# Optimization experiments

Hardware: AMD Instinct MI355X
Metric: run time of the kernel (lower is better)

## Reference

```python
import jax, jax.numpy as jnp
import numpy as np

E = 1024
H = 16
HD = E // H


def _shift(pos_score):
    # Transformer-XL relative shift trick. pos_score: [B,H,Q,K]
    B, nH, Q, K = pos_score.shape
    zeros = jnp.zeros((B, nH, Q, 1), pos_score.dtype)
    padded = jnp.concatenate([zeros, pos_score], axis=-1)  # [B,H,Q,K+1]
    padded = padded.reshape(B, nH, K + 1, Q)
    return padded[:, :, 1:].reshape(B, nH, Q, K)


def setup_inputs() -> dict:
    key = jax.random.key(0)
    ks = jax.random.split(key, 14)
    B, S = 2, 1024
    s = 1.0 / np.sqrt(E)
    inp = {
        "query": jax.random.normal(ks[0], (B, S, E), jnp.float32),
        "key": jax.random.normal(ks[1], (B, S, E), jnp.float32),
        "value": jax.random.normal(ks[2], (B, S, E), jnp.float32),
        "pos_embedding": jax.random.normal(ks[3], (B, S, E), jnp.float32),
        "Wq": jax.random.normal(ks[4], (E, E), jnp.float32) * s,
        "bq": jnp.zeros((E,), jnp.float32),
        "Wk": jax.random.normal(ks[5], (E, E), jnp.float32) * s,
        "bk": jnp.zeros((E,), jnp.float32),
        "Wv": jax.random.normal(ks[6], (E, E), jnp.float32) * s,
        "bv": jnp.zeros((E,), jnp.float32),
        "Wp": jax.random.normal(ks[7], (E, E), jnp.float32) * s,
        "U": jax.random.normal(ks[8], (H, HD), jnp.float32) * s,
        "V": jax.random.normal(ks[9], (H, HD), jnp.float32) * s,
        "Wo": jax.random.normal(ks[10], (E, E), jnp.float32) * s,
        "bo": jnp.zeros((E,), jnp.float32),
    }
    return inp


def reference(query, key, value, pos_embedding, Wq, bq, Wk, bk, Wv, bv, Wp, U, V, Wo, bo):
    B, Q, _ = query.shape
    K = key.shape[1]
    d = jnp.asarray(np.sqrt(E), query.dtype)

    q = (query @ Wq + bq).reshape(B, Q, H, HD)
    k = (key @ Wk + bk).reshape(B, K, H, HD)
    v = (value @ Wv + bv).reshape(B, K, H, HD)
    R = (pos_embedding @ Wp).reshape(B, -1, H, HD)

    content_score = jnp.einsum('bqhd,bkhd->bhqk', q + U, k)
    position_score = jnp.einsum('bqhd,bkhd->bhqk', q + V, R)
    position_score = _shift(position_score)
    attention_score = (content_score + position_score) / d  # no softmax in original

    # NOTE: faithful to original einsum 'bhqk,bvhd->bqhd' where k and v are
    # both contracted independently (sums scores over k, values over v).
    alpha = jnp.einsum('bhqk,bvhd->bqhd', attention_score, v).reshape(B, Q, E)
    return alpha @ Wo + bo
```

## Files before the change

kernel.cpp:

```cpp
#include <hip/hip_runtime.h>
#include <cstddef>
#include <cstdint>

#define E_ 1024
#define H_ 16
#define HD_ 64
#define B_ 2
#define S_ 1024
#define NSEG 64
#define SEGLEN (S_/NSEG)
#define CHUNKS 64
#define CHLEN (S_/CHUNKS)
#define SCALE 0.03125f

typedef __attribute__((ext_vector_type(8))) short bf16x8;
typedef __attribute__((ext_vector_type(4))) float f32x4;

__device__ __forceinline__ unsigned short f2bf_rne(float x) {
  uint32_t u = __float_as_uint(x);
  uint32_t r = u + 0x7FFFu + ((u >> 16) & 1u);
  return (unsigned short)(r >> 16);
}
__device__ __forceinline__ float bf2f(unsigned short h) {
  return __uint_as_float(((uint32_t)h) << 16);
}
__device__ __forceinline__ void gload_lds16(const void* g, void* l) {
  __builtin_amdgcn_global_load_lds(
      (const __attribute__((address_space(1))) void*)g,
      (__attribute__((address_space(3))) void*)l, 16, 0, 0);
}

__global__ __launch_bounds__(256) void kA_segsum(
    const float* __restrict__ pos, float* __restrict__ seg) {
  int idx = blockIdx.x*256 + threadIdx.x;
  int e = idx % E_;
  int g = (idx / E_) % NSEG;
  int b = idx / (E_*NSEG);
  const float* p = pos + ((size_t)(b*S_ + g*SEGLEN))*E_ + e;
  float s = 0.f;
  #pragma unroll
  for (int i = 0; i < SEGLEN; ++i) s += p[(size_t)i*E_];
  seg[(b*NSEG + g)*E_ + e] = s;
}

__global__ __launch_bounds__(256) void kB_scan_split(
    const float* __restrict__ pos, const float* __restrict__ seg,
    unsigned short* __restrict__ Ap) {
  int idx = blockIdx.x*256 + threadIdx.x;
  int e = idx % E_;
  int g = (idx / E_) % NSEG;
  int b = idx / (E_*NSEG);
  float run = 0.f;
  for (int gp = 0; gp < g; ++gp) run += seg[(b*NSEG + gp)*E_ + e];
  const float* p = pos + ((size_t)(b*S_ + g*SEGLEN))*E_ + e;
  #pragma unroll
  for (int i = 0; i < SEGLEN; ++i) {
    run += p[(size_t)i*E_];
    size_t row = (size_t)(b*S_ + g*SEGLEN + i);
    unsigned short hb = f2bf_rne(run);
    float lf = run - bf2f(hb);
    Ap[row*2048 + e]        = hb;
    Ap[row*2048 + 1024 + e] = f2bf_rne(lf);
  }
}

__global__ __launch_bounds__(256) void kC_split_q(
    const float* __restrict__ q, unsigned short* __restrict__ Aq) {
  int idx = blockIdx.x*256 + threadIdx.x;
  int e4 = idx & 255;
  int r  = idx >> 8;
  float4 v = ((const float4*)q)[idx];
  float xs[4] = {v.x, v.y, v.z, v.w};
  ushort4 hi, lo;
  unsigned short hb; float lf;
  hb = f2bf_rne(xs[0]); lf = xs[0]-bf2f(hb); hi.x = hb; lo.x = f2bf_rne(lf);
  hb = f2bf_rne(xs[1]); lf = xs[1]-bf2f(hb); hi.y = hb; lo.y = f2bf_rne(lf);
  hb = f2bf_rne(xs[2]); lf = xs[2]-bf2f(hb); hi.z = hb; lo.z = f2bf_rne(lf);
  hb = f2bf_rne(xs[3]); lf = xs[3]-bf2f(hb); hi.w = hb; lo.w = f2bf_rne(lf);
  *(ushort4*)&Aq[(size_t)r*2048 + e4*4]        = hi;
  *(ushort4*)&Aq[(size_t)r*2048 + 1024 + e4*4] = lo;
}

__global__ __launch_bounds__(256) void kD_splitW(
    const float* __restrict__ Wq, const float* __restrict__ Wp,
    unsigned short* __restrict__ Btq, unsigned short* __restrict__ Btp) {
  __shared__ float tile[32][33];
  const float* W = blockIdx.z ? Wp : Wq;
  unsigned short* Bt = blockIdx.z ? Btp : Btq;
  int nt = blockIdx.x, kt = blockIdx.y;
  int t = threadIdx.x;
  int lr = t >> 3;
  int lc = (t & 7) * 4;
  float4 v = *(const float4*)&W[(size_t)(kt*32 + lr)*E_ + nt*32 + lc];
  tile[lr][lc+0] = v.x; tile[lr][lc+1] = v.y;
  tile[lr][lc+2] = v.z; tile[lr][lc+3] = v.w;
  __syncthreads();
  int n = nt*32 + lr;
  ushort4 hi, lo;
  unsigned short hb; float lf; float x;
  x = tile[lc+0][lr]; hb = f2bf_rne(x); lf = x-bf2f(hb); hi.x = hb; lo.x = f2bf_rne(lf);
  x = tile[lc+1][lr]; hb = f2bf_rne(x); lf = x-bf2f(hb); hi.y = hb; lo.y = f2bf_rne(lf);
  x = tile[lc+2][lr]; hb = f2bf_rne(x); lf = x-bf2f(hb); hi.z = hb; lo.z = f2bf_rne(lf);
  x = tile[lc+3][lr]; hb = f2bf_rne(x); lf = x-bf2f(hb); hi.w = hb; lo.w = f2bf_rne(lf);
  *(ushort4*)&Bt[(size_t)n*2048 + kt*32 + lc]        = hi;
  *(ushort4*)&Bt[(size_t)n*2048 + 1024 + kt*32 + lc] = lo;
}

__global__ __launch_bounds__(256) void k1_colsum_partial(
    const float* __restrict__ key, const float* __restrict__ value,
    float* __restrict__ pk, float* __restrict__ pv) {
  int idx = blockIdx.x*256 + threadIdx.x;
  int e = idx % E_;
  int c = (idx / E_) % CHUNKS;
  int b = idx / (E_*CHUNKS);
  const float* kp = key   + ((size_t)(b*S_ + c*CHLEN))*E_ + e;
  const float* vp = value + ((size_t)(b*S_ + c*CHLEN))*E_ + e;
  float sk = 0.f, sv = 0.f;
  #pragma unroll
  for (int s = 0; s < CHLEN; ++s) {
    sk += kp[(size_t)s*E_];
    sv += vp[(size_t)s*E_];
  }
  pk[(b*CHUNKS + c)*E_ + e] = sk;
  pv[(b*CHUNKS + c)*E_ + e] = sv;
}

__global__ __launch_bounds__(256) void k2a_colsum(
    const float* __restrict__ pk, const float* __restrict__ pv,
    float* __restrict__ colsum) {
  int idx = blockIdx.x*256 + threadIdx.x;
  int e = idx & 1023;
  int b = (idx >> 10) & 1;
  int j = idx >> 11;
  const float* p = j ? pv : pk;
  float s = 0.f;
  #pragma unroll 8
  for (int c = 0; c < CHUNKS; ++c) s += p[(b*CHUNKS + c)*E_ + e];
  colsum[idx] = s;
}

__global__ __launch_bounds__(256) void k2b_gemv(
    const float* __restrict__ colsum, const float* __restrict__ Wk,
    const float* __restrict__ Wv, float* __restrict__ partial) {
  int j     = blockIdx.z;
  int slice = blockIdx.y;
  int n     = blockIdx.x*256 + threadIdx.x;
  const float* W  = j ? Wv : Wk;
  const float* cs = colsum + j*2048;
  float a0 = 0.f, a1 = 0.f;
  int e0 = slice*64;
  #pragma unroll 8
  for (int i = 0; i < 64; ++i) {
    int e = e0 + i;
    float w = W[(size_t)e*E_ + n];
    a0 += cs[e] * w;
    a1 += cs[1024 + e] * w;
  }
  partial[(size_t)((j*16 + slice)*2 + 0)*E_ + n] = a0;
  partial[(size_t)((j*16 + slice)*2 + 1)*E_ + n] = a1;
}

__global__ __launch_bounds__(256) void k2c_reduce(
    const float* __restrict__ partial, const float* __restrict__ bk,
    const float* __restrict__ bv, float* __restrict__ ksum,
    float* __restrict__ vsum) {
  int idx = blockIdx.x*256 + threadIdx.x;
  int n = idx & 1023;
  int b = (idx >> 10) & 1;
  int j = idx >> 11;
  const float* base = partial + (size_t)(j*32 + b)*E_ + n;
  float s = 0.f;
  #pragma unroll
  for (int sl = 0; sl < 16; ++sl) s += base[(size_t)sl*2*E_];
  s += (float)S_ * (j ? bv[n] : bk[n]);
  (j ? vsum : ksum)[b*E_ + n] = s;
}

__global__ __launch_bounds__(256) void k3_wv(
    const float* __restrict__ vsum, const float* __restrict__ Wo,
    float* __restrict__ WV) {
  int idx = blockIdx.x*256 + threadIdx.x;
  int n = idx % E_;
  int h = (idx / E_) % H_;
  int b = idx / (E_*H_);
  float acc = 0.f;
  #pragma unroll 8
  for (int d = 0; d < HD_; ++d)
    acc += vsum[b*E_ + h*HD_ + d] * Wo[(size_t)(h*HD_ + d)*E_ + n];
  WV[idx] = acc;
}

#define GNT 48
__global__ __launch_bounds__(256, 2) void kG_gemm(
    const unsigned short* __restrict__ Aq, const unsigned short* __restrict__ Btq,
    const float* __restrict__ bq,
    const unsigned short* __restrict__ Ap, const unsigned short* __restrict__ Btp,
    float* __restrict__ Cq, float* __restrict__ Cp) {
  __shared__ __align__(128) char lds[49152];
  const int t = threadIdx.x;
  const int lane = t & 63;
  const int wm = (t >> 6) >> 1;
  const int wn = (t >> 6) & 1;
  const int bn = blockIdx.x, bm = blockIdx.y;

  const unsigned short* A; const unsigned short* Bt;
  const float* bias; float* C;
  if (blockIdx.z == 0) { A = Aq; Bt = Btq; bias = bq;      C = Cq; }
  else                 { A = Ap; Bt = Btp; bias = nullptr; C = Cp; }

  const unsigned short* asrc[4];
  const unsigned short* bsrc[2];
  #pragma unroll
  for (int i = 0; i < 4; ++i) {
    int L = i*4096 + t*16;
    int row = L >> 7, bir = L & 127;
    int sw = bir ^ ((row & 7) << 4);
    asrc[i] = A + (size_t)(bm*128 + row)*2048 + (sw >> 1);
  }
  #pragma unroll
  for (int i = 0; i < 2; ++i) {
    int L = i*4096 + t*16;
    int row = L >> 7, bir = L & 127;
    int sw = bir ^ ((row & 7) << 4);
    bsrc[i] = Bt + (size_t)(bn*64 + row)*2048 + (sw >> 1);
  }
  int aoff[2][4], boff[2][2];
  #pragma unroll
  for (int ks = 0; ks < 2; ++ks) {
    int k0b = (ks*32 + (lane >> 4)*8) * 2;
    #pragma unroll
    for (int mi = 0; mi < 4; ++mi) {
      int row = wm*64 + mi*16 + (lane & 15);
      aoff[ks][mi] = row*128 + (k0b ^ ((row & 7) << 4));
    }
    #pragma unroll
    for (int ni = 0; ni < 2; ++ni) {
      int rown = wn*32 + ni*16 + (lane & 15);
      boff[ks][ni] = rown*128 + (k0b ^ ((rown & 7) << 4));
    }
  }

  f32x4 acc[4][2] = {};

  auto stage = [&](int buf, int kt) {
    int ak = (kt < 32) ? kt : kt - 32;
    int bk = (kt < 16) ? kt : kt - 16;
    char* Ab = lds + buf*16384;
    char* Bb = lds + 32768 + buf*8192;
    #pragma unroll
    for (int i = 0; i < 4; ++i)
      gload_lds16(asrc[i] + ak*64, Ab + i*4096 + t*16);
    #pragma unroll
    for (int i = 0; i < 2; ++i)
      gload_lds16(bsrc[i] + bk*64, Bb + i*4096 + t*16);
  };

  stage(0, 0);
  __syncthreads();
  int cur = 0;
  for (int kt = 0; kt < GNT; ++kt) {
    if (kt + 1 < GNT) stage(cur ^ 1, kt + 1);
    const char* Ab = lds + cur*16384;
    const char* Bb = lds + 32768 + cur*8192;
    bf16x8 af[2][4], bf_[2][2];
    #pragma unroll
    for (int ks = 0; ks < 2; ++ks) {
      #pragma unroll
      for (int mi = 0; mi < 4; ++mi)
        af[ks][mi] = *(const bf16x8*)(Ab + aoff[ks][mi]);
      #pragma unroll
      for (int ni = 0; ni < 2; ++ni)
        bf_[ks][ni] = *(const bf16x8*)(Bb + boff[ks][ni]);
    }
    #pragma unroll
    for (int ks = 0; ks < 2; ++ks)
      #pragma unroll
      for (int mi = 0; mi < 4; ++mi)
        #pragma unroll
        for (int ni = 0; ni < 2; ++ni)
          acc[mi][ni] = __builtin_amdgcn_mfma_f32_16x16x32_bf16(
              af[ks][mi], bf_[ks][ni], acc[mi][ni], 0, 0, 0);
    __syncthreads();
    cur ^= 1;
  }

  #pragma unroll
  for (int mi = 0; mi < 4; ++mi) {
    #pragma unroll
    for (int ni = 0; ni < 2; ++ni) {
      int col  = bn*64 + wn*32 + ni*16 + (lane & 15);
      int row0 = bm*128 + wm*64 + mi*16 + (lane >> 4)*4;
      float badd = bias ? bias[col] : 0.f;
      #pragma unroll
      for (int j = 0; j < 4; ++j)
        C[(size_t)(row0 + j)*E_ + col] = acc[mi][ni][j] + badd;
    }
  }
}

__global__ __launch_bounds__(256) void k6_rs(
    const float* __restrict__ qp, const float* __restrict__ Rpre,
    const float* __restrict__ ksum, const float* __restrict__ U,
    const float* __restrict__ V, float* __restrict__ rs) {
  int w    = blockIdx.x*4 + (threadIdx.x >> 6);
  int lane = threadIdx.x & 63;
  int q = w % S_;
  int h = (w / S_) % H_;
  int b = w / (S_*H_);
  int he = h*HD_ + lane;
  float qv0  = qp[((size_t)(b*S_ + q))*E_ + he];
  float u    = U[he], vv = V[he];
  float ks   = ksum[b*E_ + he];
  float rtot = Rpre[((size_t)(b*S_ + (S_-1)))*E_ + he];
  float tail = rtot;
  if (q <= S_-2) tail -= Rpre[((size_t)(b*S_ + (S_-2-q)))*E_ + he];
  float p = (qv0 + u)*ks + (qv0 + vv)*tail;
  if (q <= S_-3) {
    float qv1 = qp[((size_t)(b*S_ + q + 1))*E_ + he];
    float hd  = Rpre[((size_t)(b*S_ + (S_-3-q)))*E_ + he];
    p += (qv1 + vv)*hd;
  }
  #pragma unroll
  for (int off = 32; off >= 1; off >>= 1)
    p += __shfl_xor(p, off);
  if (lane == 0) rs[(b*H_ + h)*S_ + q] = p * SCALE;
}

__global__ __launch_bounds__(256) void k7_out(
    const float* __restrict__ rs, const float* __restrict__ WV,
    const float* __restrict__ bo, float* __restrict__ out) {
  int idx = blockIdx.x*256 + threadIdx.x;
  int n = idx % E_;
  int q = (idx / E_) % S_;
  int b = idx / (E_*S_);
  float acc = bo[n];
  #pragma unroll
  for (int h = 0; h < H_; ++h)
    acc += rs[(b*H_ + h)*S_ + q] * WV[((size_t)(b*H_ + h))*E_ + n];
  out[idx] = acc;
}

extern "C" void kernel_launch(void* const* d_in, const int* in_sizes, int n_in,
                              void* d_out, int out_size, void* d_ws, size_t ws_size,
                              hipStream_t stream) {
  const float* query = (const float*)d_in[0];
  const float* key   = (const float*)d_in[1];
  const float* value = (const float*)d_in[2];
  const float* pos   = (const float*)d_in[3];
  const float* Wq = (const float*)d_in[4];
  const float* bq = (const float*)d_in[5];
  const float* Wk = (const float*)d_in[6];
  const float* bk = (const float*)d_in[7];
  const float* Wv = (const float*)d_in[8];
  const float* bv = (const float*)d_in[9];
  const float* Wp = (const float*)d_in[10];
  const float* U  = (const float*)d_in[11];
  const float* V  = (const float*)d_in[12];
  const float* Wo = (const float*)d_in[13];
  const float* bo = (const float*)d_in[14];
  float* out = (float*)d_out;
  char* wsb = (char*)d_ws;

  unsigned short* Aqs = (unsigned short*)(wsb);
  unsigned short* Aps = (unsigned short*)(wsb + (8ull<<20));
  unsigned short* Btq = (unsigned short*)(wsb + (16ull<<20));
  unsigned short* Btp = (unsigned short*)(wsb + (20ull<<20));
  float* Rpre  = (float*)(wsb + (24ull<<20));
  char*  smallb = wsb + (32ull<<20);
  float* seg   = (float*)(smallb);
  float* pk    = (float*)(smallb + (512ull<<10));
  float* pv    = (float*)(smallb + (1024ull<<10));
  float* ksum  = (float*)(smallb + (1536ull<<10));
  float* vsum  = (float*)(smallb + (1544ull<<10));
  float* WVb   = (float*)(smallb + (1552ull<<10));
  float* rs    = (float*)(smallb + (1680ull<<10));
  float* qproj = out;
  float* colsum  = seg;
  float* partial = seg + 4096;

  hipLaunchKernelGGL(kA_segsum, dim3(B_*NSEG*E_/256), dim3(256), 0, stream, pos, seg);
  hipLaunchKernelGGL(kB_scan_split, dim3(B_*NSEG*E_/256), dim3(256), 0, stream, pos, seg, Aps);
  hipLaunchKernelGGL(kC_split_q, dim3(B_*S_*E_/4/256), dim3(256), 0, stream, query, Aqs);
  hipLaunchKernelGGL(kD_splitW, dim3(32, 32, 2), dim3(256), 0, stream, Wq, Wp, Btq, Btp);
  hipLaunchKernelGGL(k1_colsum_partial, dim3(B_*CHUNKS*E_/256), dim3(256), 0, stream,
                     key, value, pk, pv);
  hipLaunchKernelGGL(k2a_colsum, dim3(16), dim3(256), 0, stream, pk, pv, colsum);
  hipLaunchKernelGGL(k2b_gemv, dim3(4, 16, 2), dim3(256), 0, stream,
                     colsum, Wk, Wv, partial);
  hipLaunchKernelGGL(k2c_reduce, dim3(16), dim3(256), 0, stream,
                     partial, bk, bv, ksum, vsum);
  hipLaunchKernelGGL(k3_wv, dim3(B_*H_*E_/256), dim3(256), 0, stream, vsum, Wo, WVb);
  hipLaunchKernelGGL(kG_gemm, dim3(E_/64, B_*S_/128, 2), dim3(256), 0, stream,
                     Aqs, Btq, bq, Aps, Btp, qproj, Rpre);
  hipLaunchKernelGGL(k6_rs, dim3(B_*H_*S_/4), dim3(256), 0, stream,
                     qproj, Rpre, ksum, U, V, rs);
  hipLaunchKernelGGL(k7_out, dim3(B_*S_*E_/256), dim3(256), 0, stream,
                     rs, WVb, bo, out);
}
```

Measured before the change: 211.8 us.

## Merge independent preprocessing kernels into fused multi-role launches with atomic reduction

Collapses ten small launches into four by giving different block-index ranges different roles: segment sums, query split, weight split and key/value column sums share one launch, and scan plus colsum share another. The gemv partial reduction is replaced by atomicAdd into ksum/vsum, which are pre-initialised with the bias terms. The WV product is folded into the GEMM launch, and the GEMM block ids are remapped for locality. This removes launch gaps and serial dependencies, at the cost of nondeterministic atomic summation order and mixed-role blocks sharing one resource footprint.

```diff
diff --git a/kernel.cpp b/kernel.cpp
--- a/kernel.cpp
+++ b/kernel.cpp
@@ -30,121 +30,126 @@
       (__attribute__((address_space(3))) void*)l, 16, 0, 0);
 }
 
-__global__ __launch_bounds__(256) void kA_segsum(
-    const float* __restrict__ pos, float* __restrict__ seg) {
-  int idx = blockIdx.x*256 + threadIdx.x;
-  int e = idx % E_;
-  int g = (idx / E_) % NSEG;
-  int b = idx / (E_*NSEG);
-  const float* p = pos + ((size_t)(b*S_ + g*SEGLEN))*E_ + e;
-  float s = 0.f;
-  #pragma unroll
-  for (int i = 0; i < SEGLEN; ++i) s += p[(size_t)i*E_];
-  seg[(b*NSEG + g)*E_ + e] = s;
-}
-
-__global__ __launch_bounds__(256) void kB_scan_split(
-    const float* __restrict__ pos, const float* __restrict__ seg,
-    unsigned short* __restrict__ Ap) {
-  int idx = blockIdx.x*256 + threadIdx.x;
-  int e = idx % E_;
-  int g = (idx / E_) % NSEG;
-  int b = idx / (E_*NSEG);
-  float run = 0.f;
-  for (int gp = 0; gp < g; ++gp) run += seg[(b*NSEG + gp)*E_ + e];
-  const float* p = pos + ((size_t)(b*S_ + g*SEGLEN))*E_ + e;
-  #pragma unroll
-  for (int i = 0; i < SEGLEN; ++i) {
-    run += p[(size_t)i*E_];
-    size_t row = (size_t)(b*S_ + g*SEGLEN + i);
-    unsigned short hb = f2bf_rne(run);
-    float lf = run - bf2f(hb);
-    Ap[row*2048 + e]        = hb;
-    Ap[row*2048 + 1024 + e] = f2bf_rne(lf);
-  }
-}
-
-__global__ __launch_bounds__(256) void kC_split_q(
-    const float* __restrict__ q, unsigned short* __restrict__ Aq) {
-  int idx = blockIdx.x*256 + threadIdx.x;
-  int e4 = idx & 255;
-  int r  = idx >> 8;
-  float4 v = ((const float4*)q)[idx];
-  float xs[4] = {v.x, v.y, v.z, v.w};
-  ushort4 hi, lo;
-  unsigned short hb; float lf;
-  hb = f2bf_rne(xs[0]); lf = xs[0]-bf2f(hb); hi.x = hb; lo.x = f2bf_rne(lf);
-  hb = f2bf_rne(xs[1]); lf = xs[1]-bf2f(hb); hi.y = hb; lo.y = f2bf_rne(lf);
-  hb = f2bf_rne(xs[2]); lf = xs[2]-bf2f(hb); hi.z = hb; lo.z = f2bf_rne(lf);
-  hb = f2bf_rne(xs[3]); lf = xs[3]-bf2f(hb); hi.w = hb; lo.w = f2bf_rne(lf);
-  *(ushort4*)&Aq[(size_t)r*2048 + e4*4]        = hi;
-  *(ushort4*)&Aq[(size_t)r*2048 + 1024 + e4*4] = lo;
-}
-
-__global__ __launch_bounds__(256) void kD_splitW(
-    const float* __restrict__ Wq, const float* __restrict__ Wp,
+__global__ __launch_bounds__(256) void kP1(
+    const float* __restrict__ query, const float* __restrict__ pos,
+    const float* __restrict__ key,   const float* __restrict__ value,
+    const float* __restrict__ Wq,    const float* __restrict__ Wp,
+    float* __restrict__ seg, unsigned short* __restrict__ Aq,
+    float* __restrict__ pk, float* __restrict__ pv,
     unsigned short* __restrict__ Btq, unsigned short* __restrict__ Btp) {
   __shared__ float tile[32][33];
-  const float* W = blockIdx.z ? Wp : Wq;
-  unsigned short* Bt = blockIdx.z ? Btp : Btq;
-  int nt = blockIdx.x, kt = blockIdx.y;
+  int bid = blockIdx.x;
   int t = threadIdx.x;
-  int lr = t >> 3;
-  int lc = (t & 7) * 4;
-  float4 v = *(const float4*)&W[(size_t)(kt*32 + lr)*E_ + nt*32 + lc];
-  tile[lr][lc+0] = v.x; tile[lr][lc+1] = v.y;
-  tile[lr][lc+2] = v.z; tile[lr][lc+3] = v.w;
-  __syncthreads();
-  int n = nt*32 + lr;
-  ushort4 hi, lo;
-  unsigned short hb; float lf; float x;
-  x = tile[lc+0][lr]; hb = f2bf_rne(x); lf = x-bf2f(hb); hi.x = hb; lo.x = f2bf_rne(lf);
-  x = tile[lc+1][lr]; hb = f2bf_rne(x); lf = x-bf2f(hb); hi.y = hb; lo.y = f2bf_rne(lf);
-  x = tile[lc+2][lr]; hb = f2bf_rne(x); lf = x-bf2f(hb); hi.z = hb; lo.z = f2bf_rne(lf);
-  x = tile[lc+3][lr]; hb = f2bf_rne(x); lf = x-bf2f(hb); hi.w = hb; lo.w = f2bf_rne(lf);
-  *(ushort4*)&Bt[(size_t)n*2048 + kt*32 + lc]        = hi;
-  *(ushort4*)&Bt[(size_t)n*2048 + 1024 + kt*32 + lc] = lo;
-}
-
-__global__ __launch_bounds__(256) void k1_colsum_partial(
-    const float* __restrict__ key, const float* __restrict__ value,
-    float* __restrict__ pk, float* __restrict__ pv) {
-  int idx = blockIdx.x*256 + threadIdx.x;
-  int e = idx % E_;
-  int c = (idx / E_) % CHUNKS;
-  int b = idx / (E_*CHUNKS);
-  const float* kp = key   + ((size_t)(b*S_ + c*CHLEN))*E_ + e;
-  const float* vp = value + ((size_t)(b*S_ + c*CHLEN))*E_ + e;
-  float sk = 0.f, sv = 0.f;
-  #pragma unroll
-  for (int s = 0; s < CHLEN; ++s) {
-    sk += kp[(size_t)s*E_];
-    sv += vp[(size_t)s*E_];
-  }
-  pk[(b*CHUNKS + c)*E_ + e] = sk;
-  pv[(b*CHUNKS + c)*E_ + e] = sv;
-}
-
-__global__ __launch_bounds__(256) void k2a_colsum(
+  if (bid < 512) {
+    int idx = bid*256 + t;
+    int e = idx % E_;
+    int g = (idx / E_) % NSEG;
+    int b = idx / (E_*NSEG);
+    const float* p = pos + ((size_t)(b*S_ + g*SEGLEN))*E_ + e;
+    float s = 0.f;
+    #pragma unroll
+    for (int i = 0; i < SEGLEN; ++i) s += p[(size_t)i*E_];
+    seg[(b*NSEG + g)*E_ + e] = s;
+  } else if (bid < 2560) {
+    int idx = (bid-512)*256 + t;
+    int e4 = idx & 255;
+    int r  = idx >> 8;
+    float4 v = ((const float4*)query)[idx];
+    float xs[4] = {v.x, v.y, v.z, v.w};
+    ushort4 hi, lo;
+    unsigned short hb; float lf;
+    hb = f2bf_rne(xs[0]); lf = xs[0]-bf2f(hb); hi.x = hb; lo.x = f2bf_rne(lf);
+    hb = f2bf_rne(xs[1]); lf = xs[1]-bf2f(hb); hi.y = hb; lo.y = f2bf_rne(lf);
+    hb = f2bf_rne(xs[2]); lf = xs[2]-bf2f(hb); hi.z = hb; lo.z = f2bf_rne(lf);
+    hb = f2bf_rne(xs[3]); lf = xs[3]-bf2f(hb); hi.w = hb; lo.w = f2bf_rne(lf);
+    *(ushort4*)&Aq[(size_t)r*2048 + e4*4]        = hi;
+    *(ushort4*)&Aq[(size_t)r*2048 + 1024 + e4*4] = lo;
+  } else if (bid < 4608) {
+    int f = bid - 2560;
+    int nt = f & 31, kt = (f >> 5) & 31, z = f >> 10;
+    const float* W = z ? Wp : Wq;
+    unsigned short* Bt = z ? Btp : Btq;
+    int lr = t >> 3;
+    int lc = (t & 7) * 4;
+    float4 v = *(const float4*)&W[(size_t)(kt*32 + lr)*E_ + nt*32 + lc];
+    tile[lr][lc+0] = v.x; tile[lr][lc+1] = v.y;
+    tile[lr][lc+2] = v.z; tile[lr][lc+3] = v.w;
+    __syncthreads();
+    int n = nt*32 + lr;
+    ushort4 hi, lo;
+    unsigned short hb; float lf; float x;
+    x = tile[lc+0][lr]; hb = f2bf_rne(x); lf = x-bf2f(hb); hi.x = hb; lo.x = f2bf_rne(lf);
+    x = tile[lc+1][lr]; hb = f2bf_rne(x); lf = x-bf2f(hb); hi.y = hb; lo.y = f2bf_rne(lf);
+    x = tile[lc+2][lr]; hb = f2bf_rne(x); lf = x-bf2f(hb); hi.z = hb; lo.z = f2bf_rne(lf);
+    x = tile[lc+3][lr]; hb = f2bf_rne(x); lf = x-bf2f(hb); hi.w = hb; lo.w = f2bf_rne(lf);
+    *(ushort4*)&Bt[(size_t)n*2048 + kt*32 + lc]        = hi;
+    *(ushort4*)&Bt[(size_t)n*2048 + 1024 + kt*32 + lc] = lo;
+  } else {
+    int idx = (bid-4608)*256 + t;
+    int e = idx % E_;
+    int c = (idx / E_) % CHUNKS;
+    int b = idx / (E_*CHUNKS);
+    const float* kp = key   + ((size_t)(b*S_ + c*CHLEN))*E_ + e;
+    const float* vp = value + ((size_t)(b*S_ + c*CHLEN))*E_ + e;
+    float sk = 0.f, sv = 0.f;
+    #pragma unroll
+    for (int s = 0; s < CHLEN; ++s) {
+      sk += kp[(size_t)s*E_];
+      sv += vp[(size_t)s*E_];
+    }
+    pk[(b*CHUNKS + c)*E_ + e] = sk;
+    pv[(b*CHUNKS + c)*E_ + e] = sv;
+  }
+}
+
+__global__ __launch_bounds__(256) void kP2(
+    const float* __restrict__ pos, const float* __restrict__ seg,
+    unsigned short* __restrict__ Ap,
     const float* __restrict__ pk, const float* __restrict__ pv,
-    float* __restrict__ colsum) {
-  int idx = blockIdx.x*256 + threadIdx.x;
-  int e = idx & 1023;
-  int b = (idx >> 10) & 1;
-  int j = idx >> 11;
-  const float* p = j ? pv : pk;
-  float s = 0.f;
-  #pragma unroll 8
-  for (int c = 0; c < CHUNKS; ++c) s += p[(b*CHUNKS + c)*E_ + e];
-  colsum[idx] = s;
-}
-
-__global__ __launch_bounds__(256) void k2b_gemv(
+    const float* __restrict__ bk, const float* __restrict__ bv,
+    float* __restrict__ colsum, float* __restrict__ ksum,
+    float* __restrict__ vsum) {
+  int bid = blockIdx.x;
+  int t = threadIdx.x;
+  if (bid < 512) {
+    int idx = bid*256 + t;
+    int e = idx % E_;
+    int g = (idx / E_) % NSEG;
+    int b = idx / (E_*NSEG);
+    float run = 0.f;
+    for (int gp = 0; gp < g; ++gp) run += seg[(b*NSEG + gp)*E_ + e];
+    const float* p = pos + ((size_t)(b*S_ + g*SEGLEN))*E_ + e;
+    #pragma unroll
+    for (int i = 0; i < SEGLEN; ++i) {
+      run += p[(size_t)i*E_];
+      size_t row = (size_t)(b*S_ + g*SEGLEN + i);
+      unsigned short hb = f2bf_rne(run);
+      float lf = run - bf2f(hb);
+      Ap[row*2048 + e]        = hb;
+      Ap[row*2048 + 1024 + e] = f2bf_rne(lf);
+    }
+  } else {
+    int idx = (bid-512)*256 + t;
+    int e = idx & 1023;
+    int b = (idx >> 10) & 1;
+    int j = idx >> 11;
+    const float* p = j ? pv : pk;
+    float s = 0.f;
+    #pragma unroll 8
+    for (int c = 0; c < CHUNKS; ++c) s += p[(b*CHUNKS + c)*E_ + e];
+    colsum[idx] = s;
+    (j ? vsum : ksum)[b*E_ + e] = (float)S_ * (j ? bv : bk)[e];
+  }
+}
+
+__global__ __launch_bounds__(256) void kP3(
     const float* __restrict__ colsum, const float* __restrict__ Wk,
-    const float* __restrict__ Wv, float* __restrict__ partial) {
-  int j     = blockIdx.z;
-  int slice = blockIdx.y;
-  int n     = blockIdx.x*256 + threadIdx.x;
+    const float* __restrict__ Wv, float* __restrict__ ksum,
+    float* __restrict__ vsum) {
+  int f = blockIdx.x;
+  int j     = f >> 6;
+  int slice = (f >> 2) & 15;
+  int n     = (f & 3)*256 + threadIdx.x;
   const float* W  = j ? Wv : Wk;
   const float* cs = colsum + j*2048;
   float a0 = 0.f, a1 = 0.f;
@@ -156,57 +161,47 @@
     a0 += cs[e] * w;
     a1 += cs[1024 + e] * w;
   }
-  partial[(size_t)((j*16 + slice)*2 + 0)*E_ + n] = a0;
-  partial[(size_t)((j*16 + slice)*2 + 1)*E_ + n] = a1;
-}
-
-__global__ __launch_bounds__(256) void k2c_reduce(
-    const float* __restrict__ partial, const float* __restrict__ bk,
-    const float* __restrict__ bv, float* __restrict__ ksum,
-    float* __restrict__ vsum) {
-  int idx = blockIdx.x*256 + threadIdx.x;
-  int n = idx & 1023;
-  int b = (idx >> 10) & 1;
-  int j = idx >> 11;
-  const float* base = partial + (size_t)(j*32 + b)*E_ + n;
-  float s = 0.f;
-  #pragma unroll
-  for (int sl = 0; sl < 16; ++sl) s += base[(size_t)sl*2*E_];
-  s += (float)S_ * (j ? bv[n] : bk[n]);
-  (j ? vsum : ksum)[b*E_ + n] = s;
-}
-
-__global__ __launch_bounds__(256) void k3_wv(
-    const float* __restrict__ vsum, const float* __restrict__ Wo,
-    float* __restrict__ WV) {
-  int idx = blockIdx.x*256 + threadIdx.x;
-  int n = idx % E_;
-  int h = (idx / E_) % H_;
-  int b = idx / (E_*H_);
-  float acc = 0.f;
-  #pragma unroll 8
-  for (int d = 0; d < HD_; ++d)
-    acc += vsum[b*E_ + h*HD_ + d] * Wo[(size_t)(h*HD_ + d)*E_ + n];
-  WV[idx] = acc;
+  float* out = j ? vsum : ksum;
+  atomicAdd(&out[n], a0);
+  atomicAdd(&out[E_ + n], a1);
 }
 
 #define GNT 48
-__global__ __launch_bounds__(256, 2) void kG_gemm(
+__global__ __launch_bounds__(256, 2) void kP4(
     const unsigned short* __restrict__ Aq, const unsigned short* __restrict__ Btq,
     const float* __restrict__ bq,
     const unsigned short* __restrict__ Ap, const unsigned short* __restrict__ Btp,
-    float* __restrict__ Cq, float* __restrict__ Cp) {
+    float* __restrict__ Cq, float* __restrict__ Cp,
+    const float* __restrict__ vsum, const float* __restrict__ Wo,
+    float* __restrict__ WV) {
   __shared__ __align__(128) char lds[49152];
+  int bid = blockIdx.x;
   const int t = threadIdx.x;
+  if (bid >= 512) {
+    int idx = (bid-512)*256 + t;
+    int n = idx % E_;
+    int h = (idx / E_) % H_;
+    int b = idx / (E_*H_);
+    float acc = 0.f;
+    #pragma unroll 8
+    for (int d = 0; d < HD_; ++d)
+      acc += vsum[b*E_ + h*HD_ + d] * Wo[(size_t)(h*HD_ + d)*E_ + n];
+    WV[idx] = acc;
+    return;
+  }
+  int wg = bid;
+  int newid = (wg & 7)*64 + (wg >> 3);
+  int z  = newid >> 8;
+  int bm = (newid >> 4) & 15;
+  int bn = newid & 15;
   const int lane = t & 63;
   const int wm = (t >> 6) >> 1;
   const int wn = (t >> 6) & 1;
-  const int bn = blockIdx.x, bm = blockIdx.y;
 
   const unsigned short* A; const unsigned short* Bt;
   const float* bias; float* C;
-  if (blockIdx.z == 0) { A = Aq; Bt = Btq; bias = bq;      C = Cq; }
-  else                 { A = Ap; Bt = Btp; bias = nullptr; C = Cp; }
+  if (z == 0) { A = Aq; Bt = Btq; bias = bq;      C = Cq; }
+  else        { A = Ap; Bt = Btp; bias = nullptr; C = Cp; }
 
   const unsigned short* asrc[4];
   const unsigned short* bsrc[2];
@@ -375,23 +370,17 @@
   float* WVb   = (float*)(smallb + (1552ull<<10));
   float* rs    = (float*)(smallb + (1680ull<<10));
   float* qproj = out;
-  float* colsum  = seg;
-  float* partial = seg + 4096;
-
-  hipLaunchKernelGGL(kA_segsum, dim3(B_*NSEG*E_/256), dim3(256), 0, stream, pos, seg);
-  hipLaunchKernelGGL(kB_scan_split, dim3(B_*NSEG*E_/256), dim3(256), 0, stream, pos, seg, Aps);
-  hipLaunchKernelGGL(kC_split_q, dim3(B_*S_*E_/4/256), dim3(256), 0, stream, query, Aqs);
-  hipLaunchKernelGGL(kD_splitW, dim3(32, 32, 2), dim3(256), 0, stream, Wq, Wp, Btq, Btp);
-  hipLaunchKernelGGL(k1_colsum_partial, dim3(B_*CHUNKS*E_/256), dim3(256), 0, stream,
-                     key, value, pk, pv);
-  hipLaunchKernelGGL(k2a_colsum, dim3(16), dim3(256), 0, stream, pk, pv, colsum);
-  hipLaunchKernelGGL(k2b_gemv, dim3(4, 16, 2), dim3(256), 0, stream,
-                     colsum, Wk, Wv, partial);
-  hipLaunchKernelGGL(k2c_reduce, dim3(16), dim3(256), 0, stream,
-                     partial, bk, bv, ksum, vsum);
-  hipLaunchKernelGGL(k3_wv, dim3(B_*H_*E_/256), dim3(256), 0, stream, vsum, Wo, WVb);
-  hipLaunchKernelGGL(kG_gemm, dim3(E_/64, B_*S_/128, 2), dim3(256), 0, stream,
-                     Aqs, Btq, bq, Aps, Btp, qproj, Rpre);
+  float* colsum = (float*)(smallb + (1808ull<<10));
+
+  hipLaunchKernelGGL(kP1, dim3(5120), dim3(256), 0, stream,
+                     query, pos, key, value, Wq, Wp,
+                     seg, Aqs, pk, pv, Btq, Btp);
+  hipLaunchKernelGGL(kP2, dim3(528), dim3(256), 0, stream,
+                     pos, seg, Aps, pk, pv, bk, bv, colsum, ksum, vsum);
+  hipLaunchKernelGGL(kP3, dim3(128), dim3(256), 0, stream,
+                     colsum, Wk, Wv, ksum, vsum);
+  hipLaunchKernelGGL(kP4, dim3(640), dim3(256), 0, stream,
+                     Aqs, Btq, bq, Aps, Btp, qproj, Rpre, vsum, Wo, WVb);
   hipLaunchKernelGGL(k6_rs, dim3(B_*H_*S_/4), dim3(256), 0, stream,
                      qproj, Rpre, ksum, U, V, rs);
   hipLaunchKernelGGL(k7_out, dim3(B_*S_*E_/256), dim3(256), 0, stream,
```

Result: faster. 191.5 us (-9.6%).
